# Kernel optimization log

Measured on AMD Instinct MI355X. Metric: run time of the kernel, lower is better.

Reference implementation:

```python
import jax, jax.numpy as jnp
import numpy as np

B, D, CLASSES = 8192, 128, 5

def setup_inputs() -> dict:
    key = jax.random.key(0)
    ks = jax.random.split(key, 7)
    d2 = 2 * D
    return {
        "left": jax.random.normal(ks[0], (B, D), jnp.float32),
        "right": jax.random.normal(ks[1], (B, D), jnp.float32),
        "V": jax.random.normal(ks[2], (d2, d2, D), jnp.float32) * 0.02,
        "W_w": jax.random.normal(ks[3], (D, d2), jnp.float32) * 0.02,
        "W_b": jax.random.normal(ks[4], (D,), jnp.float32) * 0.02,
        "Ws_w": jax.random.normal(ks[5], (CLASSES, D), jnp.float32) * 0.02,
        "Ws_b": jax.random.normal(ks[6], (CLASSES,), jnp.float32) * 0.02,
    }

def reference(left, right, V, W_w, W_b, Ws_w, Ws_b):
    # phrase: [B, 2d]
    phrase = jnp.concatenate([left, right], axis=1)
    d2 = phrase.shape[1]
    d = V.shape[2]
    # Fused bilinear tensor product: result[b,k] = sum_ij phrase[b,i] V[i,j,k] phrase[b,j]
    # One GEMM: (B,2d) @ (2d, 2d*d) -> (B,2d,d), then contract j with phrase.
    pv = (phrase @ V.reshape(d2, d2 * d)).reshape(-1, d2, d)   # [B,2d,d]
    tp = jnp.einsum('bj,bjk->bk', phrase, pv)                  # [B,d]
    # node: tanh(tensorProduct + W(phrase))
    h = jnp.tanh(tp + phrase @ W_w.T + W_b)                    # [B,d]
    # sentiment: log_softmax(Ws(h))
    logits = h @ Ws_w.T + Ws_b                                 # [B,classes]
    return jax.nn.log_softmax(logits, axis=1)
```

## Files before the change

### kernel.cpp

```cpp
#include <hip/hip_runtime.h>
#include <hip/hip_fp16.h>
#include <math.h>

typedef _Float16 f16x8 __attribute__((ext_vector_type(8)));
typedef _Float16 f16x4 __attribute__((ext_vector_type(4)));
typedef float f32x4 __attribute__((ext_vector_type(4)));

#define DD     128
#define D2     256
#define NB     8192
#define NCLS   5
#define KSPLIT 8
#define BM     128
#define PPAD   258
#define NSB    36
#define SB_BYTES  262144u
#define TAIL_OFF  (36u * 262144u)
#define PART_OFF  (10u * 1048576u)

__global__ void prep_vt(const float* __restrict__ V, const float* __restrict__ Ww,
                        _Float16* __restrict__ Vt) {
    int t = blockIdx.x * 256 + threadIdx.x;
    int u = t >> 7;
    int n = t & 127;
    f16x8 v;
    if (u < NSB * 128) {
        int s = u >> 7, g = u & 127;
        int bi = 0, rem = s;
        while (rem >= 8 - bi) { rem -= 8 - bi; ++bi; }
        int bj = bi + rem;
        int i  = bi * 32 + (g >> 2);
        int j0 = bj * 32 + (g & 3) * 8;
        if (bi == bj) {
            #pragma unroll
            for (int e = 0; e < 8; ++e)
                v[e] = (_Float16)V[((size_t)i * 256 + j0 + e) * 128 + n];
        } else {
            #pragma unroll
            for (int e = 0; e < 8; ++e)
                v[e] = (_Float16)(V[((size_t)i * 256 + j0 + e) * 128 + n]
                                + V[((size_t)(j0 + e) * 256 + i) * 128 + n]);
        }
    } else {
        int g = u - NSB * 128;
        int j0 = g * 8;
        #pragma unroll
        for (int e = 0; e < 8; ++e)
            v[e] = (_Float16)Ww[n * D2 + j0 + e];
    }
    *(f16x8*)(Vt + (size_t)u * 1024 + n * 8) = v;
}

__global__ __launch_bounds__(256, 2) void gemm_bilinear(
        const float* __restrict__ left, const float* __restrict__ right,
        const _Float16* __restrict__ Vt, float* __restrict__ part) {
    __shared__ _Float16 P[BM][PPAD];

    const int bid = blockIdx.x;
    const int ks  = bid & 7;
    const int m0  = (bid >> 3) * BM;
    const int tid = threadIdx.x;

    for (int it = 0; it < 32; ++it) {
        int f4  = it * 256 + tid;
        int row = f4 >> 6;
        int col = (f4 & 63) * 4;
        const float* src = (col < DD) ? (left  + (size_t)(m0 + row) * DD + col)
                                      : (right + (size_t)(m0 + row) * DD + (col - DD));
        float4 x = *(const float4*)src;
        f16x4 hv;
        hv[0] = (_Float16)x.x; hv[1] = (_Float16)x.y;
        hv[2] = (_Float16)x.z; hv[3] = (_Float16)x.w;
        *(f16x4*)&P[row][col] = hv;
    }
    __syncthreads();

    const int lane = tid & 63;
    const int wid  = tid >> 6;
    const int wm   = wid >> 1, wn = wid & 1;
    const int l15  = lane & 15, lg = lane >> 4;
    const int rowb = wm * 64;
    const int coln = wn * 64;

    f32x4 acc[4][4];
    #pragma unroll
    for (int u = 0; u < 4; ++u)
        #pragma unroll
        for (int w = 0; w < 4; ++w)
            acc[u][w] = (f32x4){0.f, 0.f, 0.f, 0.f};

    const unsigned lane_nbyte = (unsigned)((coln + l15) * 16);
    #define LDV(off) (*(const f16x8*)((const char*)Vt + (off)))

    #define LOADB(BUF)                                                                    \
        asm volatile("global_load_dwordx4 %0, %4, %5\n\t"                                 \
                     "global_load_dwordx4 %1, %4, %5 offset:256\n\t"                      \
                     "global_load_dwordx4 %2, %4, %5 offset:512\n\t"                      \
                     "global_load_dwordx4 %3, %4, %5 offset:768"                          \
            : "=&v"(BUF[0]), "=&v"(BUF[1]), "=&v"(BUF[2]), "=&v"(BUF[3])                  \
            : "v"(voff), "s"(Vt));                                                        \
        voff += 8192u;

    #define WAITN(N)                                                                      \
        asm volatile("s_waitcnt vmcnt(" #N ")");                                          \
        __builtin_amdgcn_sched_barrier(0);

    #define MFMA_CLUSTER(BUF, IBE)                                                        \
        __builtin_amdgcn_s_setprio(1);                                                    \
        _Pragma("unroll")                                                                 \
        for (int mr = 0; mr < 4; ++mr) {                                                  \
            const _Float16 sc = pis[mr][IBE];                                             \
            const f16x8 a = pj[mr] * sc;                                                  \
            _Pragma("unroll")                                                             \
            for (int nr = 0; nr < 4; ++nr)                                                \
                acc[mr][nr] = __builtin_amdgcn_mfma_f32_16x16x32_f16(a, BUF[nr], acc[mr][nr], 0, 0, 0); \
        }                                                                                 \
        __builtin_amdgcn_s_setprio(0);

    #define LOAD_PIS(IBC)                                                                 \
        f16x8 pis[4];                                                                     \
        _Pragma("unroll")                                                                 \
        for (int mr = 0; mr < 4; ++mr)                                                    \
            pis[mr] = *(const f16x8*)&P[rowb + mr * 16 + l15][bi * 32 + (IBC) * 8];

    #pragma unroll 1
    for (int si = 0; si < 5; ++si) {
        int s, ibcS, ibcE;
        if (si < 4) { s = ks * 4 + si;      ibcS = 0;            ibcE = 4; }
        else        { s = 32 + (ks >> 1);   ibcS = (ks & 1) * 2; ibcE = ibcS + 2; }

        int bi = 0, rem = s;
        while (rem >= 8 - bi) { rem -= 8 - bi; ++bi; }
        const int bj = bi + rem;

        f16x8 pj[4];
        #pragma unroll
        for (int mr = 0; mr < 4; ++mr)
            pj[mr] = *(const f16x8*)&P[rowb + mr * 16 + l15][bj * 32 + lg * 8];

        unsigned voff = lane_nbyte + (unsigned)s * SB_BYTES + (unsigned)(lg * 2048)
                      + (unsigned)(ibcS * 65536);

        f16x8 B0[4], B1[4], B2[4], B3[4];
        LOADB(B0)
        LOADB(B1)

        #pragma unroll 1
        for (int ibc = ibcS; ibc < ibcE - 1; ++ibc) {
            LOAD_PIS(ibc)
            LOADB(B2)  WAITN(8)  MFMA_CLUSTER(B0, 0)
            LOADB(B3)  WAITN(8)  MFMA_CLUSTER(B1, 1)
            LOADB(B0)  WAITN(8)  MFMA_CLUSTER(B2, 2)
            LOADB(B1)  WAITN(8)  MFMA_CLUSTER(B3, 3)
            LOADB(B2)  WAITN(8)  MFMA_CLUSTER(B0, 4)
            LOADB(B3)  WAITN(8)  MFMA_CLUSTER(B1, 5)
            LOADB(B0)  WAITN(8)  MFMA_CLUSTER(B2, 6)
            LOADB(B1)  WAITN(8)  MFMA_CLUSTER(B3, 7)
        }

        {
            LOAD_PIS(ibcE - 1)
            LOADB(B2)  WAITN(8)  MFMA_CLUSTER(B0, 0)
            LOADB(B3)  WAITN(8)  MFMA_CLUSTER(B1, 1)
            LOADB(B0)  WAITN(8)  MFMA_CLUSTER(B2, 2)
            LOADB(B1)  WAITN(8)  MFMA_CLUSTER(B3, 3)
            LOADB(B2)  WAITN(8)  MFMA_CLUSTER(B0, 4)
            LOADB(B3)  WAITN(8)  MFMA_CLUSTER(B1, 5)
                       WAITN(4)  MFMA_CLUSTER(B2, 6)
                       WAITN(0)  MFMA_CLUSTER(B3, 7)
        }
    }

    if (ks == KSPLIT - 1) {
        #pragma unroll 1
        for (int jc = 0; jc < 8; ++jc) {
            unsigned voff = TAIL_OFF + (unsigned)((jc * 4 + lg) * 2048) + lane_nbyte;
            f16x8 bfr[4];
            #pragma unroll
            for (int nr = 0; nr < 4; ++nr) bfr[nr] = LDV(voff + nr * 256);
            #pragma unroll
            for (int mr = 0; mr < 4; ++mr) {
                const f16x8 a = *(const f16x8*)&P[rowb + mr * 16 + l15][jc * 32 + lg * 8];
                #pragma unroll
                for (int nr = 0; nr < 4; ++nr)
                    acc[mr][nr] = __builtin_amdgcn_mfma_f32_16x16x32_f16(a, bfr[nr], acc[mr][nr], 0, 0, 0);
            }
        }
    }

    float* base = part + ((size_t)ks * NB + m0) * DD;
    #pragma unroll
    for (int mr = 0; mr < 4; ++mr)
        #pragma unroll
        for (int nr = 0; nr < 4; ++nr) {
            const int col = coln + nr * 16 + l15;
            #pragma unroll
            for (int q = 0; q < 4; ++q) {
                const int row = rowb + mr * 16 + lg * 4 + q;
                base[(size_t)row * DD + col] = acc[mr][nr][q];
            }
        }
}

__global__ void finish(const float* __restrict__ part, const float* __restrict__ Wb,
                       const float* __restrict__ Wsw, const float* __restrict__ Wsb,
                       float* __restrict__ out) {
    int t  = blockIdx.x * 256 + threadIdx.x;
    int b  = t >> 2;
    int kq = t & 3;
    if (b >= NB) return;
    float lg[NCLS];
    #pragma unroll
    for (int c = 0; c < NCLS; ++c) lg[c] = 0.f;

    const float* pb = part + (size_t)b * DD + kq * 32;
    #pragma unroll 1
    for (int k4 = 0; k4 < 8; ++k4) {
        float4 tt = *(const float4*)(Wb + kq * 32 + k4 * 4);
        #pragma unroll
        for (int s = 0; s < KSPLIT; ++s) {
            float4 p = *(const float4*)(pb + (size_t)s * NB * DD + k4 * 4);
            tt.x += p.x; tt.y += p.y; tt.z += p.z; tt.w += p.w;
        }
        float tq[4] = {tt.x, tt.y, tt.z, tt.w};
        #pragma unroll
        for (int q = 0; q < 4; ++q) {
            float h = tanhf(tq[q]);
            int k = kq * 32 + k4 * 4 + q;
            #pragma unroll
            for (int c = 0; c < NCLS; ++c)
                lg[c] += h * Wsw[c * DD + k];
        }
    }
    #pragma unroll
    for (int c = 0; c < NCLS; ++c) {
        lg[c] += __shfl_xor(lg[c], 1);
        lg[c] += __shfl_xor(lg[c], 2);
    }
    if (kq == 0) {
        #pragma unroll
        for (int c = 0; c < NCLS; ++c) lg[c] += Wsb[c];
        float mx = lg[0];
        #pragma unroll
        for (int c = 1; c < NCLS; ++c) mx = fmaxf(mx, lg[c]);
        float sum = 0.f;
        #pragma unroll
        for (int c = 0; c < NCLS; ++c) sum += expf(lg[c] - mx);
        float lse = logf(sum);
        #pragma unroll
        for (int c = 0; c < NCLS; ++c) out[b * NCLS + c] = lg[c] - mx - lse;
    }
}

extern "C" void kernel_launch(void* const* d_in, const int* in_sizes, int n_in,
                              void* d_out, int out_size, void* d_ws, size_t ws_size,
                              hipStream_t stream) {
    const float* left  = (const float*)d_in[0];
    const float* right = (const float*)d_in[1];
    const float* V     = (const float*)d_in[2];
    const float* Ww    = (const float*)d_in[3];
    const float* Wb    = (const float*)d_in[4];
    const float* Wsw   = (const float*)d_in[5];
    const float* Wsb   = (const float*)d_in[6];
    float* out = (float*)d_out;

    _Float16* Vt = (_Float16*)d_ws;
    float* part  = (float*)((char*)d_ws + PART_OFF);

    hipLaunchKernelGGL(prep_vt, dim3(2320), dim3(256), 0, stream, V, Ww, Vt);
    hipLaunchKernelGGL(gemm_bilinear, dim3((NB / BM) * KSPLIT), dim3(256), 0, stream,
                       left, right, Vt, part);
    hipLaunchKernelGGL(finish, dim3(NB * 4 / 256), dim3(256), 0, stream, part, Wb, Wsw, Wsb, out);
}
```

Baseline: 104.7 us.

## Switch bilinear GEMM to 32x32x16 MFMA tiles and widen finish parallelism

```diff
diff --git a/kernel.cpp b/kernel.cpp
--- a/kernel.cpp
+++ b/kernel.cpp
@@ -5,6 +5,7 @@
 typedef _Float16 f16x8 __attribute__((ext_vector_type(8)));
 typedef _Float16 f16x4 __attribute__((ext_vector_type(4)));
 typedef float f32x4 __attribute__((ext_vector_type(4)));
+typedef float f32x16 __attribute__((ext_vector_type(16)));
 
 #define DD     128
 #define D2     256
@@ -78,28 +79,30 @@
     const int lane = tid & 63;
     const int wid  = tid >> 6;
     const int wm   = wid >> 1, wn = wid & 1;
-    const int l15  = lane & 15, lg = lane >> 4;
+    const int l31  = lane & 31;
+    const int lg2  = lane >> 5;
     const int rowb = wm * 64;
     const int coln = wn * 64;
 
-    f32x4 acc[4][4];
-    #pragma unroll
-    for (int u = 0; u < 4; ++u)
-        #pragma unroll
-        for (int w = 0; w < 4; ++w)
-            acc[u][w] = (f32x4){0.f, 0.f, 0.f, 0.f};
-
-    const unsigned lane_nbyte = (unsigned)((coln + l15) * 16);
+    f32x16 acc[2][2];
+    #pragma unroll
+    for (int u = 0; u < 2; ++u)
+        #pragma unroll
+        for (int w = 0; w < 2; ++w)
+            acc[u][w] = (f32x16){0.f,0.f,0.f,0.f,0.f,0.f,0.f,0.f,
+                                 0.f,0.f,0.f,0.f,0.f,0.f,0.f,0.f};
+
+    const unsigned lane_byte = (unsigned)(lg2 * 2048 + (coln + l31) * 16);
     #define LDV(off) (*(const f16x8*)((const char*)Vt + (off)))
 
     #define LOADB(BUF)                                                                    \
-        asm volatile("global_load_dwordx4 %0, %4, %5\n\t"                                 \
-                     "global_load_dwordx4 %1, %4, %5 offset:256\n\t"                      \
-                     "global_load_dwordx4 %2, %4, %5 offset:512\n\t"                      \
-                     "global_load_dwordx4 %3, %4, %5 offset:768"                          \
+        asm volatile("global_load_dwordx4 %0, %4, %6\n\t"                                 \
+                     "global_load_dwordx4 %1, %4, %6 offset:512\n\t"                      \
+                     "global_load_dwordx4 %2, %5, %6\n\t"                                 \
+                     "global_load_dwordx4 %3, %5, %6 offset:512"                          \
             : "=&v"(BUF[0]), "=&v"(BUF[1]), "=&v"(BUF[2]), "=&v"(BUF[3])                  \
-            : "v"(voff), "s"(Vt));                                                        \
-        voff += 8192u;
+            : "v"(voffA), "v"(voffB), "s"(Vt));                                           \
+        voffA += 8192u; voffB += 8192u;
 
     #define WAITN(N)                                                                      \
         asm volatile("s_waitcnt vmcnt(" #N ")");                                          \
@@ -108,20 +111,22 @@
     #define MFMA_CLUSTER(BUF, IBE)                                                        \
         __builtin_amdgcn_s_setprio(1);                                                    \
         _Pragma("unroll")                                                                 \
-        for (int mr = 0; mr < 4; ++mr) {                                                  \
+        for (int mr = 0; mr < 2; ++mr) {                                                  \
             const _Float16 sc = pis[mr][IBE];                                             \
-            const f16x8 a = pj[mr] * sc;                                                  \
-            _Pragma("unroll")                                                             \
-            for (int nr = 0; nr < 4; ++nr)                                                \
-                acc[mr][nr] = __builtin_amdgcn_mfma_f32_16x16x32_f16(a, BUF[nr], acc[mr][nr], 0, 0, 0); \
+            const f16x8 a0 = pj2[mr][0] * sc;                                             \
+            const f16x8 a1 = pj2[mr][1] * sc;                                             \
+            acc[mr][0] = __builtin_amdgcn_mfma_f32_32x32x16_f16(a0, BUF[0], acc[mr][0], 0, 0, 0); \
+            acc[mr][1] = __builtin_amdgcn_mfma_f32_32x32x16_f16(a0, BUF[1], acc[mr][1], 0, 0, 0); \
+            acc[mr][0] = __builtin_amdgcn_mfma_f32_32x32x16_f16(a1, BUF[2], acc[mr][0], 0, 0, 0); \
+            acc[mr][1] = __builtin_amdgcn_mfma_f32_32x32x16_f16(a1, BUF[3], acc[mr][1], 0, 0, 0); \
         }                                                                                 \
         __builtin_amdgcn_s_setprio(0);
 
     #define LOAD_PIS(IBC)                                                                 \
-        f16x8 pis[4];                                                                     \
+        f16x8 pis[2];                                                                     \
         _Pragma("unroll")                                                                 \
-        for (int mr = 0; mr < 4; ++mr)                                                    \
-            pis[mr] = *(const f16x8*)&P[rowb + mr * 16 + l15][bi * 32 + (IBC) * 8];
+        for (int mr = 0; mr < 2; ++mr)                                                    \
+            pis[mr] = *(const f16x8*)&P[rowb + mr * 32 + l31][bi * 32 + (IBC) * 8];
 
     #pragma unroll 1
     for (int si = 0; si < 5; ++si) {
@@ -133,13 +138,15 @@
         while (rem >= 8 - bi) { rem -= 8 - bi; ++bi; }
         const int bj = bi + rem;
 
-        f16x8 pj[4];
-        #pragma unroll
-        for (int mr = 0; mr < 4; ++mr)
-            pj[mr] = *(const f16x8*)&P[rowb + mr * 16 + l15][bj * 32 + lg * 8];
-
-        unsigned voff = lane_nbyte + (unsigned)s * SB_BYTES + (unsigned)(lg * 2048)
-                      + (unsigned)(ibcS * 65536);
+        f16x8 pj2[2][2];
+        #pragma unroll
+        for (int mr = 0; mr < 2; ++mr)
+            #pragma unroll
+            for (int k16 = 0; k16 < 2; ++k16)
+                pj2[mr][k16] = *(const f16x8*)&P[rowb + mr * 32 + l31][bj * 32 + k16 * 16 + lg2 * 8];
+
+        unsigned voffA = lane_byte + (unsigned)s * SB_BYTES + (unsigned)(ibcS * 65536);
+        unsigned voffB = voffA + 4096u;
 
         f16x8 B0[4], B1[4], B2[4], B3[4];
         LOADB(B0)
@@ -174,30 +181,32 @@
     if (ks == KSPLIT - 1) {
         #pragma unroll 1
         for (int jc = 0; jc < 8; ++jc) {
-            unsigned voff = TAIL_OFF + (unsigned)((jc * 4 + lg) * 2048) + lane_nbyte;
+            unsigned vA = TAIL_OFF + (unsigned)(jc * 4) * 2048u + lane_byte;
             f16x8 bfr[4];
-            #pragma unroll
-            for (int nr = 0; nr < 4; ++nr) bfr[nr] = LDV(voff + nr * 256);
-            #pragma unroll
-            for (int mr = 0; mr < 4; ++mr) {
-                const f16x8 a = *(const f16x8*)&P[rowb + mr * 16 + l15][jc * 32 + lg * 8];
-                #pragma unroll
-                for (int nr = 0; nr < 4; ++nr)
-                    acc[mr][nr] = __builtin_amdgcn_mfma_f32_16x16x32_f16(a, bfr[nr], acc[mr][nr], 0, 0, 0);
+            bfr[0] = LDV(vA);           bfr[1] = LDV(vA + 512);
+            bfr[2] = LDV(vA + 4096);    bfr[3] = LDV(vA + 4608);
+            #pragma unroll
+            for (int mr = 0; mr < 2; ++mr) {
+                const f16x8 a0 = *(const f16x8*)&P[rowb + mr * 32 + l31][jc * 32 + lg2 * 8];
+                const f16x8 a1 = *(const f16x8*)&P[rowb + mr * 32 + l31][jc * 32 + 16 + lg2 * 8];
+                acc[mr][0] = __builtin_amdgcn_mfma_f32_32x32x16_f16(a0, bfr[0], acc[mr][0], 0, 0, 0);
+                acc[mr][1] = __builtin_amdgcn_mfma_f32_32x32x16_f16(a0, bfr[1], acc[mr][1], 0, 0, 0);
+                acc[mr][0] = __builtin_amdgcn_mfma_f32_32x32x16_f16(a1, bfr[2], acc[mr][0], 0, 0, 0);
+                acc[mr][1] = __builtin_amdgcn_mfma_f32_32x32x16_f16(a1, bfr[3], acc[mr][1], 0, 0, 0);
             }
         }
     }
 
     float* base = part + ((size_t)ks * NB + m0) * DD;
     #pragma unroll
-    for (int mr = 0; mr < 4; ++mr)
-        #pragma unroll
-        for (int nr = 0; nr < 4; ++nr) {
-            const int col = coln + nr * 16 + l15;
-            #pragma unroll
-            for (int q = 0; q < 4; ++q) {
-                const int row = rowb + mr * 16 + lg * 4 + q;
-                base[(size_t)row * DD + col] = acc[mr][nr][q];
+    for (int mr = 0; mr < 2; ++mr)
+        #pragma unroll
+        for (int nt = 0; nt < 2; ++nt) {
+            const int col = coln + nt * 32 + l31;
+            #pragma unroll
+            for (int r = 0; r < 16; ++r) {
+                const int row = rowb + mr * 32 + (r & 3) + 8 * (r >> 2) + 4 * lg2;
+                base[(size_t)row * DD + col] = acc[mr][nt][r];
             }
         }
 }
@@ -206,17 +215,17 @@
                        const float* __restrict__ Wsw, const float* __restrict__ Wsb,
                        float* __restrict__ out) {
     int t  = blockIdx.x * 256 + threadIdx.x;
-    int b  = t >> 2;
-    int kq = t & 3;
+    int b  = t >> 3;
+    int kq = t & 7;
     if (b >= NB) return;
     float lg[NCLS];
     #pragma unroll
     for (int c = 0; c < NCLS; ++c) lg[c] = 0.f;
 
-    const float* pb = part + (size_t)b * DD + kq * 32;
+    const float* pb = part + (size_t)b * DD + kq * 16;
     #pragma unroll 1
-    for (int k4 = 0; k4 < 8; ++k4) {
-        float4 tt = *(const float4*)(Wb + kq * 32 + k4 * 4);
+    for (int k4 = 0; k4 < 4; ++k4) {
+        float4 tt = *(const float4*)(Wb + kq * 16 + k4 * 4);
         #pragma unroll
         for (int s = 0; s < KSPLIT; ++s) {
             float4 p = *(const float4*)(pb + (size_t)s * NB * DD + k4 * 4);
@@ -226,7 +235,7 @@
         #pragma unroll
         for (int q = 0; q < 4; ++q) {
             float h = tanhf(tq[q]);
-            int k = kq * 32 + k4 * 4 + q;
+            int k = kq * 16 + k4 * 4 + q;
             #pragma unroll
             for (int c = 0; c < NCLS; ++c)
                 lg[c] += h * Wsw[c * DD + k];
@@ -236,6 +245,7 @@
     for (int c = 0; c < NCLS; ++c) {
         lg[c] += __shfl_xor(lg[c], 1);
         lg[c] += __shfl_xor(lg[c], 2);
+        lg[c] += __shfl_xor(lg[c], 4);
     }
     if (kq == 0) {
         #pragma unroll
@@ -270,5 +280,5 @@
     hipLaunchKernelGGL(prep_vt, dim3(2320), dim3(256), 0, stream, V, Ww, Vt);
     hipLaunchKernelGGL(gemm_bilinear, dim3((NB / BM) * KSPLIT), dim3(256), 0, stream,
                        left, right, Vt, part);
-    hipLaunchKernelGGL(finish, dim3(NB * 4 / 256), dim3(256), 0, stream, part, Wb, Wsw, Wsb, out);
-}
+    hipLaunchKernelGGL(finish, dim3(NB * 8 / 256), dim3(256), 0, stream, part, Wb, Wsw, Wsb, out);
+}
```

New measurement: 104.8 us. Within noise of the previous version (+0.1%).
